# Kernel optimization log

Measured on AMD Instinct MI355X. Metric: run time of the kernel, lower is better.

Reference implementation:

```python
import jax, jax.numpy as jnp
import numpy as np
from jax import lax

D = 1024          # d_model
ORDER = 2         # hyena order
FILT = 64         # filter_order (implicit MLP width)
EMB = 3           # positional embedding dim (default)
INNER = D * (ORDER + 1)
DF = D * (ORDER - 1)   # filter d_model
L_MAX = 2048


def setup_inputs() -> dict:
    key = jax.random.key(0)
    ks = jax.random.split(key, 16)
    s = 0.02
    return {
        "u": jax.random.normal(ks[0], (4, L_MAX, D), jnp.float32),
        "in_w": jax.random.normal(ks[1], (D, INNER), jnp.float32) * s,
        "in_b": jnp.zeros((INNER,), jnp.float32),
        "short_w": jax.random.normal(ks[2], (INNER, 3), jnp.float32) * 0.3,
        "short_b": jnp.zeros((INNER,), jnp.float32),
        "mlp_w1": jax.random.normal(ks[3], (EMB, FILT), jnp.float32) * 0.3,
        "mlp_b1": jnp.zeros((FILT,), jnp.float32),
        "mlp_w2": jax.random.normal(ks[4], (FILT, FILT), jnp.float32) * 0.1,
        "mlp_b2": jnp.zeros((FILT,), jnp.float32),
        "mlp_w3": jax.random.normal(ks[5], (FILT, FILT), jnp.float32) * 0.1,
        "mlp_b3": jnp.zeros((FILT,), jnp.float32),
        "mlp_wo": jax.random.normal(ks[6], (FILT, DF), jnp.float32) * 0.1,
        "freq": jnp.ones((1, FILT), jnp.float32),       # shared Sin freq (w=1)
        "filt_bias": jax.random.normal(ks[7], (DF,), jnp.float32),
        "out_w": jax.random.normal(ks[8], (D, D), jnp.float32) * s,
        "out_b": jnp.zeros((D,), jnp.float32),
    }


def _pos_emb(L):
    # PositionalEmbedding(emb_dim=3): t, real/imag of exp(-i f w), bands=(3-1)//2=1
    t = jnp.linspace(0.0, 1.0, L)[:, None]                      # (L,1)
    tr = jnp.linspace(0.0, L - 1.0, L)[:, None]
    w = 2.0 * np.pi * tr / L                                    # (L,1)
    f = jnp.array([1e-4], jnp.float32)[None, :]                  # bands=1
    z = jnp.concatenate([t, jnp.cos(f * w), -jnp.sin(f * w)], axis=-1)  # (L,3)
    return z, t


def _decay(t):
    # ExponentialModulation: target=1e-2, fast=0.3, slow=1.5, shift=0
    max_d = np.log(1e-2) / 0.3
    min_d = np.log(1e-2) / 1.5
    deltas = jnp.linspace(min_d, max_d, DF)[None, :]             # (1,DF)
    return jnp.exp(-t * jnp.abs(deltas))                         # (L,DF)


def reference(u, in_w, in_b, short_w, short_b, mlp_w1, mlp_b1, mlp_w2, mlp_b2,
              mlp_w3, mlp_b3, mlp_wo, freq, filt_bias, out_w, out_b):
    B, L, _ = u.shape
    # in_proj: b l d -> b l (3d) -> b (3d) l
    up = jnp.einsum('bld,de->ble', u, in_w) + in_b
    up = up.transpose(0, 2, 1)                                   # (B, INNER, L)
    # depthwise short conv, kernel 3, padding 2 both sides, then [:L]
    uc = lax.conv_general_dilated(up, short_w[:, None, :], (1,), [(2, 2)],
                                  feature_group_count=INNER,
                                  dimension_numbers=('NCH', 'OIH', 'NCH'))
    uc = uc[..., :L] + short_b[None, :, None]
    x0, x1, v = uc[:, :D], uc[:, D:2 * D], uc[:, 2 * D:]
    # implicit long filter k(L): pos-emb -> Sin MLP (shared freq) -> modulation
    z, t = _pos_emb(L)
    h = jnp.sin(freq * (z @ mlp_w1 + mlp_b1))
    h = jnp.sin(freq * (h @ mlp_w2 + mlp_b2))
    h = jnp.sin(freq * (h @ mlp_w3 + mlp_b3))
    h = h @ mlp_wo                                               # (L, DF)
    k = (h * _decay(t)).T                                        # (DF, L) == (D, L) for order=2
    # hyena recurrence: order-1 = 1 gated fft-conv step
    vx = v * x1                                                  # (B, D, L)
    n = 2 * L
    y = jnp.fft.irfft(jnp.fft.rfft(vx, n=n) * jnp.fft.rfft(k, n=n), n=n)[..., :L]
    v = y + vx * filt_bias[None, :, None]
    # final gate + out_proj
    yv = (v * x0).transpose(0, 2, 1)                             # (B, L, D)
    return jnp.einsum('bld,de->ble', yv, out_w) + out_b
```

## Files before the change

### kernel.cpp

```cpp
#include <hip/hip_runtime.h>
#include <math.h>

#define M_PIf 3.14159265358979323846f
#define MIND (-3.0701134573253936f)
#define MAXD (-15.350567286626968f)

typedef __attribute__((ext_vector_type(8))) _Float16 f16x8;
typedef __attribute__((ext_vector_type(4))) float f32x4;
typedef __attribute__((ext_vector_type(8))) unsigned short u16x8;

#define GLDS(g, l) __builtin_amdgcn_global_load_lds(                         \
    (const __attribute__((address_space(1))) void*)(g),                      \
    (__attribute__((address_space(3))) void*)(l), 16, 0, 0)

__device__ __forceinline__ unsigned short f2h(float x) {
    return __builtin_bit_cast(unsigned short, (_Float16)x);
}
__device__ __forceinline__ float h2f(unsigned short h) {
    return (float)__builtin_bit_cast(_Float16, h);
}

__global__ __launch_bounds__(256) void prep_kernel(
    const float* __restrict__ u, unsigned short* __restrict__ uh,
    const float* __restrict__ in_w, unsigned short* __restrict__ w1t,
    const float* __restrict__ w1, const float* __restrict__ b1,
    const float* __restrict__ w2, const float* __restrict__ b2,
    const float* __restrict__ w3, const float* __restrict__ b3,
    const float* __restrict__ wo, const float* __restrict__ freq,
    float* __restrict__ kbuf)
{
    __shared__ char sm[4352];
    const int bid = blockIdx.x;
    const int tid = threadIdx.x;

    if (bid < 8192) {
        const int i = bid * 256 + tid;
        float4 v = ((const float4*)u)[i];
        ushort4 h;
        h.x = f2h(v.x); h.y = f2h(v.y); h.z = f2h(v.z); h.w = f2h(v.w);
        ((ushort4*)uh)[i] = h;
    } else if (bid < 11264) {
        float (*t)[33] = (float(*)[33])sm;
        const int idx = bid - 8192;
        const int bx = idx % 96, by = idx / 96;
        const int r0 = by * 32, c0 = bx * 32;
        const int tx = tid & 31, ty = tid >> 5;
#pragma unroll
        for (int q = 0; q < 4; ++q) {
            int r = ty + q * 8;
            t[r][tx] = in_w[(size_t)(r0 + r) * 3072 + c0 + tx];
        }
        __syncthreads();
#pragma unroll
        for (int q = 0; q < 4; ++q) {
            int cc = ty + q * 8;
            w1t[(size_t)(c0 + cc) * 1024 + r0 + tx] = f2h(t[tx][cc]);
        }
    } else {
        float (*ha)[65] = (float(*)[65])sm;
        float (*hb)[65] = (float(*)[65])(sm + 2080);
        const int l0 = (bid - 11264) * 8;
        const int uu = tid & 63, lq = tid >> 6;
#pragma unroll
        for (int p = 0; p < 2; ++p) {
            int ll = lq + p * 4;
            int l = l0 + ll;
            float t = (float)l * (1.0f / 2047.0f);
            float ang = 1e-4f * (2.0f * M_PIf) * ((float)l / 2048.0f);
            float pre = t * w1[uu] + cosf(ang) * w1[64 + uu] - sinf(ang) * w1[128 + uu] + b1[uu];
            ha[ll][uu] = sinf(freq[uu] * pre);
        }
        __syncthreads();
#pragma unroll
        for (int p = 0; p < 2; ++p) {
            int ll = lq + p * 4;
            float s = b2[uu];
#pragma unroll
            for (int i = 0; i < 64; ++i) s += ha[ll][i] * w2[i * 64 + uu];
            hb[ll][uu] = sinf(freq[uu] * s);
        }
        __syncthreads();
#pragma unroll
        for (int p = 0; p < 2; ++p) {
            int ll = lq + p * 4;
            float s = b3[uu];
#pragma unroll
            for (int i = 0; i < 64; ++i) s += hb[ll][i] * w3[i * 64 + uu];
            ha[ll][uu] = sinf(freq[uu] * s);
        }
        __syncthreads();

        float acc[4][8] = {};
        for (int i = 0; i < 64; ++i) {
            float wv[4];
#pragma unroll
            for (int q = 0; q < 4; ++q) wv[q] = wo[i * 1024 + tid + 256 * q];
#pragma unroll
            for (int l = 0; l < 8; ++l) {
                float hv = ha[l][i];
#pragma unroll
                for (int q = 0; q < 4; ++q) acc[q][l] += hv * wv[q];
            }
        }
        const float span = (MAXD - MIND) * (1.0f / 1023.0f);
#pragma unroll
        for (int q = 0; q < 4; ++q) {
            int dd = tid + 256 * q;
            float ad = fabsf(MIND + span * (float)dd);
#pragma unroll
            for (int l = 0; l < 8; ++l) {
                float t = (float)(l0 + l) * (1.0f / 2047.0f);
                kbuf[(size_t)dd * 2048 + l0 + l] = acc[q][l] * expf(-t * ad);
            }
        }
    }
}

__global__ __launch_bounds__(256) void post_kernel(
    const unsigned short* __restrict__ yvh, unsigned short* __restrict__ yvt,
    const float* __restrict__ out_w, unsigned short* __restrict__ w2t)
{
    __shared__ char sm[8448];
    const int bid = blockIdx.x;
    const int tid = threadIdx.x;
    if (bid < 2048) {
        unsigned short (*t)[66] = (unsigned short(*)[66])sm;
        const int l0 = (bid & 31) * 64;
        const int d0 = ((bid >> 5) & 15) * 64;
        const int b  = bid >> 9;
        const int rr = tid >> 4, cc = (tid & 15) * 4;
#pragma unroll
        for (int p = 0; p < 4; ++p) {
            int r = p * 16 + rr;
            ushort4 v = *(const ushort4*)&yvh[((size_t)b * 1024 + d0 + r) * 2048 + l0 + cc];
            t[cc + 0][r] = v.x; t[cc + 1][r] = v.y; t[cc + 2][r] = v.z; t[cc + 3][r] = v.w;
        }
        __syncthreads();
#pragma unroll
        for (int p = 0; p < 4; ++p) {
            int r = p * 16 + rr;
            ushort4 o;
            o.x = t[r][cc + 0]; o.y = t[r][cc + 1]; o.z = t[r][cc + 2]; o.w = t[r][cc + 3];
            *(ushort4*)&yvt[((size_t)b * 2048 + l0 + r) * 1024 + d0 + cc] = o;
        }
    } else {
        float (*t)[33] = (float(*)[33])sm;
        const int idx = bid - 2048;
        const int bx = idx & 31, by = idx >> 5;
        const int r0 = by * 32, c0 = bx * 32;
        const int tx = tid & 31, ty = tid >> 5;
#pragma unroll
        for (int q = 0; q < 4; ++q) {
            int r = ty + q * 8;
            t[r][tx] = out_w[(size_t)(r0 + r) * 1024 + c0 + tx];
        }
        __syncthreads();
#pragma unroll
        for (int q = 0; q < 4; ++q) {
            int cc = ty + q * 8;
            w2t[(size_t)(c0 + cc) * 1024 + r0 + tx] = f2h(t[tx][cc]);
        }
    }
}

template <int TRANS_OUT>
__global__ __launch_bounds__(256, 4) void gemm_f16_kernel(
    const unsigned short* __restrict__ A, const unsigned short* __restrict__ B,
    const float* __restrict__ bias, void* __restrict__ outp)
{
    __shared__ char smem[32768];
    const int tid = threadIdx.x;
    const int wave = tid >> 6, lane = tid & 63;
    const int n0 = blockIdx.x * 128, m0 = blockIdx.y * 128;
    const int wm = wave >> 1, wn = wave & 1;

    f32x4 acc[4][4] = {};

    const int srow = lane >> 2;
    const int scol_sw = (((lane & 3) ^ ((lane >> 3) & 3))) * 16;

    auto stage = [&](int buf, int t) {
        const int k0 = t * 32;
        char* base = smem + buf * 16384;
#pragma unroll
        for (int ld = 0; ld < 2; ++ld) {
            const int rchunk = wave * 32 + ld * 16;
            const int r = rchunk + srow;
            GLDS((const char*)(A + (size_t)(m0 + r) * 1024 + k0) + scol_sw,
                 base + 0 * 8192 + rchunk * 64);
            GLDS((const char*)(B + (size_t)(n0 + r) * 1024 + k0) + scol_sw,
                 base + 1 * 8192 + rchunk * 64);
        }
    };

    stage(0, 0);
    asm volatile("s_waitcnt vmcnt(0)");
    __syncthreads();
    int cur = 0;
    const int rr = lane & 15;
    const int gg_sw = (((lane >> 4) ^ ((rr >> 1) & 3))) * 16;
    for (int t = 0; t < 32; ++t) {
        if (t < 31) stage(cur ^ 1, t + 1);
        const char* b = smem + cur * 16384;
        f16x8 ah[4], bh[4];
#pragma unroll
        for (int i = 0; i < 4; ++i) {
            ah[i] = *(const f16x8*)(b + 0 * 8192 + (wm * 64 + i * 16 + rr) * 64 + gg_sw);
            bh[i] = *(const f16x8*)(b + 1 * 8192 + (wn * 64 + i * 16 + rr) * 64 + gg_sw);
        }
#pragma unroll
        for (int i = 0; i < 4; ++i)
#pragma unroll
            for (int j = 0; j < 4; ++j)
                acc[i][j] = __builtin_amdgcn_mfma_f32_16x16x32_f16(ah[i], bh[j], acc[i][j], 0, 0, 0);
        __syncthreads();
        cur ^= 1;
    }

    const int c = lane & 15, g4 = lane >> 4;
    if (TRANS_OUT) {
        unsigned short* up = (unsigned short*)outp;
        const int bidx = m0 >> 11;
        const int lbase = (m0 & 2047) + wm * 64 + g4 * 4;
#pragma unroll
        for (int j = 0; j < 4; ++j) {
            const int e = n0 + wn * 64 + j * 16 + c;
            const float bv = bias[e];
            unsigned short* dst = up + ((size_t)bidx * 3072 + e) * 2048 + lbase;
#pragma unroll
            for (int i = 0; i < 4; ++i) {
                ushort4 o;
                o.x = f2h(acc[i][j][0] + bv);
                o.y = f2h(acc[i][j][1] + bv);
                o.z = f2h(acc[i][j][2] + bv);
                o.w = f2h(acc[i][j][3] + bv);
                *(ushort4*)(dst + i * 16) = o;
            }
        }
    } else {
        float* op = (float*)outp;
#pragma unroll
        for (int j = 0; j < 4; ++j) {
            const int col = n0 + wn * 64 + j * 16 + c;
            const float bv = bias[col];
#pragma unroll
            for (int i = 0; i < 4; ++i) {
                const int row = m0 + wm * 64 + i * 16 + g4 * 4;
#pragma unroll
                for (int r = 0; r < 4; ++r)
                    op[(size_t)(row + r) * 1024 + col] = acc[i][j][r] + bv;
            }
        }
    }
}

__device__ __forceinline__ void conv3_chunk(
    const unsigned short* __restrict__ row, int l0,
    float wa, float wb, float wc, float sbv, float out[8])
{
    f16x8 m = *(const f16x8*)(row + l0);
    float e[10];
    if (l0 > 0) {
        ushort2 p = *(const ushort2*)(row + l0 - 2);
        e[0] = h2f(p.x); e[1] = h2f(p.y);
    } else {
        e[0] = 0.f; e[1] = 0.f;
    }
#pragma unroll
    for (int i = 0; i < 8; ++i) e[2 + i] = (float)m[i];
#pragma unroll
    for (int i = 0; i < 8; ++i)
        out[i] = wa * e[i] + wb * e[i + 1] + wc * e[i + 2] + sbv;
}

__global__ __launch_bounds__(256, 4) void conv_kernel(
    const unsigned short* __restrict__ up_t, const float* __restrict__ kbuf,
    const float* __restrict__ sw, const float* __restrict__ sb,
    const float* __restrict__ fbias, unsigned short* __restrict__ yv)
{
    __shared__ char smem[27712];
#define VH(bb) ((unsigned short*)(smem + (bb) * 4608))
#define X0(bb) ((unsigned short*)(smem + 17472 + (bb) * 5120))
    int* wpk = (int*)(smem + 9216);

    const int d = blockIdx.x;
    const int bqa = blockIdx.y * 2;
    const int tid = threadIdx.x;

    const float* kr = kbuf + (size_t)d * 2048;
    for (int xc = tid * 4; xc < 2064; xc += 1024) {
        int4 w4 = {0, 0, 0, 0};
        if (xc <= 2044) {
            const float4 fv = *(const float4*)&kr[2044 - xc];
            const float e = (xc <= 2040) ? kr[2043 - xc] : 0.f;
            w4.x = (int)((unsigned)f2h(fv.w) | ((unsigned)f2h(fv.z) << 16));
            w4.y = (int)((unsigned)f2h(fv.z) | ((unsigned)f2h(fv.y) << 16));
            w4.z = (int)((unsigned)f2h(fv.y) | ((unsigned)f2h(fv.x) << 16));
            w4.w = (int)((unsigned)f2h(fv.x) | ((unsigned)f2h(e)    << 16));
        }
        *(int4*)&wpk[xc] = w4;
    }

    const float w1a = sw[(1024 + d) * 3 + 0], w1b = sw[(1024 + d) * 3 + 1], w1c = sw[(1024 + d) * 3 + 2];
    const float w2a = sw[(2048 + d) * 3 + 0], w2b = sw[(2048 + d) * 3 + 1], w2c = sw[(2048 + d) * 3 + 2];
    const float w0a = sw[d * 3 + 0], w0b = sw[d * 3 + 1], w0c = sw[d * 3 + 2];
    const float sb1 = sb[1024 + d], sb2 = sb[2048 + d], sb0 = sb[d];
    const int l0 = tid * 8;
#pragma unroll
    for (int bb = 0; bb < 2; ++bb) {
        const int b = bqa + bb;
        const unsigned short* rx1 = up_t + ((size_t)(b * 3072) + 1024 + d) * 2048;
        const unsigned short* rv  = up_t + ((size_t)(b * 3072) + 2048 + d) * 2048;
        const unsigned short* r0  = up_t + ((size_t)(b * 3072) + d) * 2048;
        float x1v[8], vv[8], x0v[8];
        conv3_chunk(rx1, l0, w1a, w1b, w1c, sb1, x1v);
        conv3_chunk(rv,  l0, w2a, w2b, w2c, sb2, vv);
        conv3_chunk(r0,  l0, w0a, w0b, w0c, sb0, x0v);
        u16x8 o;
#pragma unroll
        for (int i = 0; i < 8; ++i) o[i] = f2h(vv[i] * x1v[i]);
        *(u16x8*)(VH(bb) + 240 + l0) = o;
        const int xo = l0 + 4 * (l0 >> 4);
        ushort4 p1, p2;
        p1.x = f2h(x0v[0]); p1.y = f2h(x0v[1]); p1.z = f2h(x0v[2]); p1.w = f2h(x0v[3]);
        p2.x = f2h(x0v[4]); p2.y = f2h(x0v[5]); p2.z = f2h(x0v[6]); p2.w = f2h(x0v[7]);
        *(ushort4*)(X0(bb) + xo) = p1;
        *(ushort4*)(X0(bb) + xo + 4) = p2;
        if (tid < 30) {
            u16x8 z = {};
            *(u16x8*)(VH(bb) + tid * 8) = z;
        }
    }
    __syncthreads();

    const int wv = tid >> 6, lane = tid & 63;
    const int row = lane & 15;
    const int sseg = lane >> 4;
    f32x4 acc[2][2] = {};
#pragma unroll
    for (int gi = 0; gi < 2; ++gi) {
        const int g = gi ? (7 - wv) : wv;
        const int tmax = 8 * g + 8;
        int xA = 2031 - row + 8 * sseg;
        int xB = 224 + 256 * g + 16 * row + 8 * sseg;
        auto step = [&]() {
            int4 avh;
            avh.x = wpk[xA];     avh.y = wpk[xA + 2];
            avh.z = wpk[xA + 4]; avh.w = wpk[xA + 6];
            f16x8 ah = __builtin_bit_cast(f16x8, avh);
#pragma unroll
            for (int bb = 0; bb < 2; ++bb) {
                f16x8 bh = *(const f16x8*)(VH(bb) + xB);
                acc[gi][bb] = __builtin_amdgcn_mfma_f32_16x16x32_f16(ah, bh, acc[gi][bb], 0, 0, 0);
            }
            xA -= 32;
            xB -= 32;
        };
        for (int t = 0; t < tmax; t += 2) { step(); step(); }
    }

    const float fb = fbias[d];
#pragma unroll
    for (int gi = 0; gi < 2; ++gi) {
        const int g = gi ? (7 - wv) : wv;
        const int lb = 256 * g + 16 * row + 4 * sseg;
#pragma unroll
        for (int bb = 0; bb < 2; ++bb) {
            ushort4 vhq = *(const ushort4*)(VH(bb) + 240 + lb);
            ushort4 x0q = *(const ushort4*)(X0(bb) + lb + 4 * (lb >> 4));
            f32x4 a = acc[gi][bb];
            ushort4 o;
            o.x = f2h((a[0] + h2f(vhq.x) * fb) * h2f(x0q.x));
            o.y = f2h((a[1] + h2f(vhq.y) * fb) * h2f(x0q.y));
            o.z = f2h((a[2] + h2f(vhq.z) * fb) * h2f(x0q.z));
            o.w = f2h((a[3] + h2f(vhq.w) * fb) * h2f(x0q.w));
            *(ushort4*)&yv[((size_t)((bqa + bb) * 1024) + d) * 2048 + lb] = o;
        }
    }
#undef VH
#undef X0
}

extern "C" void kernel_launch(void* const* d_in, const int* in_sizes, int n_in,
                              void* d_out, int out_size, void* d_ws, size_t ws_size,
                              hipStream_t stream) {
    (void)in_sizes; (void)n_in; (void)out_size; (void)ws_size;
    const float* u         = (const float*)d_in[0];
    const float* in_w      = (const float*)d_in[1];
    const float* in_b      = (const float*)d_in[2];
    const float* short_w   = (const float*)d_in[3];
    const float* short_b   = (const float*)d_in[4];
    const float* mlp_w1    = (const float*)d_in[5];
    const float* mlp_b1    = (const float*)d_in[6];
    const float* mlp_w2    = (const float*)d_in[7];
    const float* mlp_b2    = (const float*)d_in[8];
    const float* mlp_w3    = (const float*)d_in[9];
    const float* mlp_b3    = (const float*)d_in[10];
    const float* mlp_wo    = (const float*)d_in[11];
    const float* freq      = (const float*)d_in[12];
    const float* filt_bias = (const float*)d_in[13];
    const float* out_w     = (const float*)d_in[14];
    const float* out_b     = (const float*)d_in[15];
    float* out = (float*)d_out;

    char* ws = (char*)d_ws;
    const size_t MB = 1024 * 1024;
    unsigned short* up_t = (unsigned short*)ws;
    unsigned short* yvh  = (unsigned short*)(ws + 48 * MB);
    unsigned short* yvt  = (unsigned short*)(ws + 64 * MB);
    unsigned short* w2t  = (unsigned short*)(ws + 80 * MB);
    float*          kbuf = (float*)(ws + 82 * MB);
    unsigned short* uh   = (unsigned short*)(ws + 90 * MB);
    unsigned short* w1t  = (unsigned short*)(ws + 106 * MB);

    hipLaunchKernelGGL(prep_kernel, dim3(11520), dim3(256), 0, stream,
                       u, uh, in_w, w1t,
                       mlp_w1, mlp_b1, mlp_w2, mlp_b2, mlp_w3, mlp_b3, mlp_wo, freq, kbuf);
    hipLaunchKernelGGL((gemm_f16_kernel<1>), dim3(24, 64), dim3(256), 0, stream,
                       uh, w1t, in_b, (void*)up_t);
    hipLaunchKernelGGL(conv_kernel, dim3(1024, 2), dim3(256), 0, stream,
                       up_t, kbuf, short_w, short_b, filt_bias, yvh);
    hipLaunchKernelGGL(post_kernel, dim3(3072), dim3(256), 0, stream,
                       yvh, yvt, out_w, w2t);
    hipLaunchKernelGGL((gemm_f16_kernel<0>), dim3(8, 64), dim3(256), 0, stream,
                       yvt, w2t, out_b, (void*)out);
}
```

Measured before the change: 176.1 us.

## Rewrite f16 GEMM as 8-wave 256x128 tile with phased LDS pipeline

Replaces the 4-wave 128x128 double-buffered GEMM with an 8-wave kernel computing 256x128 tiles over 64-wide K steps. Loads are split into half-tile phases that interleave global-to-LDS staging with MFMA work, using explicit barriers, setprio and partial vmcnt waits. The goal is to hide memory latency and reuse the B tile across more rows. The cost is 96KB of LDS per block, which allows only one block per CU, plus a hand-tuned schedule whose correctness depends on exact waitcnt counts. The epilogue must also map correctly onto the new wave layout.

```diff
diff --git a/kernel.cpp b/kernel.cpp
--- a/kernel.cpp
+++ b/kernel.cpp
@@ -164,60 +164,84 @@
 }
 
 template <int TRANS_OUT>
-__global__ __launch_bounds__(256, 4) void gemm_f16_kernel(
+__global__ __launch_bounds__(512, 1) void gemm8_f16_kernel(
     const unsigned short* __restrict__ A, const unsigned short* __restrict__ B,
     const float* __restrict__ bias, void* __restrict__ outp)
 {
-    __shared__ char smem[32768];
+    __shared__ char smem[98304];
     const int tid = threadIdx.x;
     const int wave = tid >> 6, lane = tid & 63;
-    const int n0 = blockIdx.x * 128, m0 = blockIdx.y * 128;
+    const int n0 = blockIdx.x * 128, m0 = blockIdx.y * 256;
     const int wm = wave >> 1, wn = wave & 1;
+    const int rr = lane & 15, g4 = lane >> 4;
+    const int srow4 = lane >> 2;
+    const int sswz  = ((lane & 3) ^ ((lane >> 2) & 3)) * 8;
+    const int axor  = (g4 ^ (rr & 3)) * 16;
 
     f32x4 acc[4][4] = {};
-
-    const int srow = lane >> 2;
-    const int scol_sw = (((lane & 3) ^ ((lane >> 3) & 3))) * 16;
-
-    auto stage = [&](int buf, int t) {
-        const int k0 = t * 32;
-        char* base = smem + buf * 16384;
-#pragma unroll
-        for (int ld = 0; ld < 2; ++ld) {
-            const int rchunk = wave * 32 + ld * 16;
-            const int r = rchunk + srow;
-            GLDS((const char*)(A + (size_t)(m0 + r) * 1024 + k0) + scol_sw,
-                 base + 0 * 8192 + rchunk * 64);
-            GLDS((const char*)(B + (size_t)(n0 + r) * 1024 + k0) + scol_sw,
-                 base + 1 * 8192 + rchunk * 64);
+    f16x8 bq[4];
+
+    auto stageA = [&](int bufo, int t, int kh) {
+        const int ke = t * 64 + kh * 32;
+        char* ldsb = smem + bufo + kh * 16384 + wave * 1024;
+#pragma unroll
+        for (int j = 0; j < 2; ++j) {
+            const int rg = j * 128 + wave * 16 + srow4;
+            GLDS((const char*)(A + (size_t)(m0 + rg) * 1024 + ke + sswz), ldsb + j * 8192);
         }
     };
-
-    stage(0, 0);
-    asm volatile("s_waitcnt vmcnt(0)");
+    auto stageB = [&](int bufo, int t, int kh) {
+        const int ke = t * 64 + kh * 32;
+        const int rg = wave * 16 + srow4;
+        GLDS((const char*)(B + (size_t)(n0 + rg) * 1024 + ke + sswz),
+             smem + bufo + 32768 + kh * 8192 + wave * 1024);
+    };
+
+    auto phase = [&](int bufo, int s, int h, auto stage_fn, int vm) {
+        const char* bb = smem + bufo;
+        f16x8 aq0, aq1;
+        if (h == 0) {
+#pragma unroll
+            for (int j = 0; j < 4; ++j)
+                bq[j] = *(const f16x8*)(bb + 32768 + s * 8192 + (wn * 64 + j * 16 + rr) * 64 + axor);
+        }
+        aq0 = *(const f16x8*)(bb + s * 16384 + (wm * 64 + (h * 2 + 0) * 16 + rr) * 64 + axor);
+        aq1 = *(const f16x8*)(bb + s * 16384 + (wm * 64 + (h * 2 + 1) * 16 + rr) * 64 + axor);
+        stage_fn();
+        __builtin_amdgcn_s_barrier();
+        __builtin_amdgcn_s_setprio(1);
+#pragma unroll
+        for (int j = 0; j < 4; ++j)
+            acc[h * 2 + 0][j] = __builtin_amdgcn_mfma_f32_16x16x32_f16(aq0, bq[j], acc[h * 2 + 0][j], 0, 0, 0);
+#pragma unroll
+        for (int j = 0; j < 4; ++j)
+            acc[h * 2 + 1][j] = __builtin_amdgcn_mfma_f32_16x16x32_f16(aq1, bq[j], acc[h * 2 + 1][j], 0, 0, 0);
+        __builtin_amdgcn_s_setprio(0);
+        if (vm == 1) asm volatile("s_waitcnt vmcnt(3)" ::: "memory");
+        else if (vm == 2) asm volatile("s_waitcnt vmcnt(0)" ::: "memory");
+        __builtin_amdgcn_s_barrier();
+    };
+
+    stageA(0, 0, 0); stageB(0, 0, 0);
+    stageA(0, 0, 1); stageB(0, 0, 1);
+    stageA(49152, 1, 0); stageB(49152, 1, 0);
+    asm volatile("s_waitcnt vmcnt(0)" ::: "memory");
     __syncthreads();
-    int cur = 0;
-    const int rr = lane & 15;
-    const int gg_sw = (((lane >> 4) ^ ((rr >> 1) & 3))) * 16;
-    for (int t = 0; t < 32; ++t) {
-        if (t < 31) stage(cur ^ 1, t + 1);
-        const char* b = smem + cur * 16384;
-        f16x8 ah[4], bh[4];
-#pragma unroll
-        for (int i = 0; i < 4; ++i) {
-            ah[i] = *(const f16x8*)(b + 0 * 8192 + (wm * 64 + i * 16 + rr) * 64 + gg_sw);
-            bh[i] = *(const f16x8*)(b + 1 * 8192 + (wn * 64 + i * 16 + rr) * 64 + gg_sw);
-        }
-#pragma unroll
-        for (int i = 0; i < 4; ++i)
-#pragma unroll
-            for (int j = 0; j < 4; ++j)
-                acc[i][j] = __builtin_amdgcn_mfma_f32_16x16x32_f16(ah[i], bh[j], acc[i][j], 0, 0, 0);
-        __syncthreads();
-        cur ^= 1;
-    }
-
-    const int c = lane & 15, g4 = lane >> 4;
+
+    for (int it = 0; it < 8; ++it) {
+        const int T1 = 2 * it + 1, T2 = 2 * it + 2, T3 = 2 * it + 3;
+        const int vmL = (it == 7) ? 2 : 1;
+        phase(0,     0, 0, [&] { stageA(49152, T1, 1); }, 0);
+        phase(0,     0, 1, [&] { stageB(49152, T1, 1); }, 0);
+        phase(0,     1, 0, [&] { if (T2 < 16) stageA(0, T2, 0); }, 0);
+        phase(0,     1, 1, [&] { if (T2 < 16) stageB(0, T2, 0); }, vmL);
+        phase(49152, 0, 0, [&] { if (T2 < 16) stageA(0, T2, 1); }, 0);
+        phase(49152, 0, 1, [&] { if (T2 < 16) stageB(0, T2, 1); }, 0);
+        phase(49152, 1, 0, [&] { if (T3 < 16) stageA(49152, T3, 0); }, 0);
+        phase(49152, 1, 1, [&] { if (T3 < 16) stageB(49152, T3, 0); }, vmL);
+    }
+
+    const int c = rr;
     if (TRANS_OUT) {
         unsigned short* up = (unsigned short*)outp;
         const int bidx = m0 >> 11;
@@ -416,12 +440,12 @@
     hipLaunchKernelGGL(prep_kernel, dim3(11520), dim3(256), 0, stream,
                        u, uh, in_w, w1t,
                        mlp_w1, mlp_b1, mlp_w2, mlp_b2, mlp_w3, mlp_b3, mlp_wo, freq, kbuf);
-    hipLaunchKernelGGL((gemm_f16_kernel<1>), dim3(24, 64), dim3(256), 0, stream,
+    hipLaunchKernelGGL((gemm8_f16_kernel<1>), dim3(24, 32), dim3(512), 0, stream,
                        uh, w1t, in_b, (void*)up_t);
     hipLaunchKernelGGL(conv_kernel, dim3(1024, 2), dim3(256), 0, stream,
                        up_t, kbuf, short_w, short_b, filt_bias, yvh);
     hipLaunchKernelGGL(post_kernel, dim3(3072), dim3(256), 0, stream,
                        yvh, yvt, out_w, w2t);
-    hipLaunchKernelGGL((gemm_f16_kernel<0>), dim3(8, 64), dim3(256), 0, stream,
+    hipLaunchKernelGGL((gemm8_f16_kernel<0>), dim3(8, 32), dim3(512), 0, stream,
                        yvt, w2t, out_b, (void*)out);
 }
```

New measurement: 177.5 us. About the same (+0.7%).
